# Kernel optimization log

Hardware: AMD Instinct MI355X
Metric: run time of the kernel (lower is better)

## Reference

```python
import jax, jax.numpy as jnp
import numpy as np

N = 50000
E = 800000
IN = 128
HID = 32
OUT = 32
H1, H2 = 4, 4
NEG_SLOPE = 0.2


def setup_inputs() -> dict:
    key = jax.random.key(0)
    ks = jax.random.split(key, 12)
    x = jax.random.normal(ks[0], (N, IN), dtype=jnp.float32)
    src = jax.random.randint(ks[1], (E,), 0, N, dtype=jnp.int32)
    dst = jax.random.randint(ks[2], (E,), 0, N, dtype=jnp.int32)
    s = 0.1
    # layer 1: fc (IN -> H1*HID, no bias), attn vectors (H1, HID), bias (H1*HID,)
    W1 = jax.random.normal(ks[3], (IN, H1 * HID), dtype=jnp.float32) * s
    al1 = jax.random.normal(ks[4], (H1, HID), dtype=jnp.float32) * s
    ar1 = jax.random.normal(ks[5], (H1, HID), dtype=jnp.float32) * s
    b1 = jnp.zeros((H1 * HID,), dtype=jnp.float32)
    # layer 2: fc (H1*HID -> H2*OUT, no bias)
    W2 = jax.random.normal(ks[6], (H1 * HID, H2 * OUT), dtype=jnp.float32) * s
    al2 = jax.random.normal(ks[7], (H2, OUT), dtype=jnp.float32) * s
    ar2 = jax.random.normal(ks[8], (H2, OUT), dtype=jnp.float32) * s
    b2 = jnp.zeros((H2 * OUT,), dtype=jnp.float32)
    return {"x": x, "W1": W1, "al1": al1, "ar1": ar1, "b1": b1,
            "W2": W2, "al2": al2, "ar2": ar2, "b2": b2,
            "src": src, "dst": dst}


def _gat_layer(x, W, al, ar, b, src, dst, n, h, d):
    # feat_drop is identity (eval mode)
    feat = (x @ W).reshape(n, h, d)                       # [N,H,D]
    el = jnp.einsum('nhd,hd->nh', feat, al)               # [N,H]
    er = jnp.einsum('nhd,hd->nh', feat, ar)               # [N,H]
    e = jax.nn.leaky_relu(el[src] + er[dst], NEG_SLOPE)   # [E,H] SDDMM
    # edge softmax over incoming edges of each destination node
    emax = jax.ops.segment_max(e, dst, num_segments=n)    # [N,H]
    emax = jnp.where(jnp.isfinite(emax), emax, 0.0)       # guard 0-in-degree
    w = jnp.exp(e - emax[dst])                            # [E,H]
    denom = jax.ops.segment_sum(w, dst, num_segments=n)   # [N,H]
    alpha = w / jnp.maximum(denom[dst], 1e-9)             # [E,H]; attn_drop identity
    # SpMM aggregation
    rst = jax.ops.segment_sum(feat[src] * alpha[:, :, None], dst, num_segments=n)
    # residual: in_feats == h*d for both layers -> DGL uses Identity res_fc
    rst = rst + x.reshape(n, h, d)
    rst = rst + b.reshape(1, h, d)
    return rst


def reference(x, W1, al1, ar1, b1, W2, al2, ar2, b2, src, dst):
    h = _gat_layer(x, W1, al1, ar1, b1, src, dst, N, H1, HID)
    h = jax.nn.elu(h)                                     # layer-1 activation
    h = h.reshape(N, H1 * HID)                            # flatten(1)
    h = _gat_layer(h, W2, al2, ar2, b2, src, dst, N, H2, OUT)
    return h.mean(axis=1)                                 # [N,OUT]
```

## Files before the change

kernel.cpp:

```cpp
#include <hip/hip_runtime.h>
#include <cstdint>
#include <cstddef>

#define NEG_SLOPE 0.2f

typedef __bf16 bf16x8 __attribute__((ext_vector_type(8)));
typedef float  f32x4  __attribute__((ext_vector_type(4)));

__device__ inline unsigned int bf16pair(float a, float b) {
    unsigned int ua = __float_as_uint(a), ub = __float_as_uint(b);
    ua += 0x7fffu + ((ua >> 16) & 1u);
    ub += 0x7fffu + ((ub >> 16) & 1u);
    return (ua >> 16) | (ub & 0xffff0000u);
}
__device__ inline unsigned short bf16r(float x) {
    unsigned int u = __float_as_uint(x);
    u += 0x7fffu + ((u >> 16) & 1u);
    return (unsigned short)(u >> 16);
}

__global__ __launch_bounds__(256) void prep_kernel(
    const float* __restrict__ W1, const float* __restrict__ W2,
    unsigned short* __restrict__ Wt1, unsigned short* __restrict__ Wt2,
    const int* __restrict__ dst, int* __restrict__ deg,
    int* __restrict__ rank, int E)
{
    __shared__ float tile[64][65];
    if (blockIdx.x < 8) {
        const float* W = (blockIdx.x < 4) ? W1 : W2;
        unsigned short* Wt = (blockIdx.x < 4) ? Wt1 : Wt2;
        const int tb = blockIdx.x & 3;
        const int k0 = (tb >> 1) * 64, n0 = (tb & 1) * 64;
        const int c = threadIdx.x & 63, r4 = threadIdx.x >> 6;
#pragma unroll
        for (int i = 0; i < 16; ++i) {
            const int r = i * 4 + r4;
            tile[r][c] = W[(size_t)(k0 + r) * 128 + n0 + c];
        }
        __syncthreads();
#pragma unroll
        for (int i = 0; i < 16; ++i) {
            const int nn = i * 4 + r4;
            Wt[(size_t)(n0 + nn) * 128 + k0 + c] = bf16r(tile[c][nn]);
        }
        return;
    }
    const int bid = blockIdx.x - 8;
    const int e4 = (bid * 256 + threadIdx.x) * 4;
    if (e4 + 4 <= E) {
        const int4 d = *(const int4*)&dst[e4];
        int4 r;
        r.x = atomicAdd(&deg[d.x], 1);
        r.y = atomicAdd(&deg[d.y], 1);
        r.z = atomicAdd(&deg[d.z], 1);
        r.w = atomicAdd(&deg[d.w], 1);
        *(int4*)&rank[e4] = r;
    } else {
        for (int e = e4; e < E; ++e) rank[e] = atomicAdd(&deg[dst[e]], 1);
    }
}

template <bool XBF16>
__global__ __launch_bounds__(256, 4) void gemm_attn_kernel(
    const void* __restrict__ Xv, const unsigned short* __restrict__ Wt,
    const float* __restrict__ al, const float* __restrict__ ar,
    unsigned short* __restrict__ feat16, float* __restrict__ el,
    float* __restrict__ er, int n)
{
    __shared__ unsigned short sX[64][136];
    __shared__ unsigned short sF[64][136];

    const int t = threadIdx.x;
    const int rowbase = blockIdx.x * 64;

    if (XBF16) {
        const unsigned short* X = (const unsigned short*)Xv;
#pragma unroll
        for (int i = 0; i < 4; ++i) {
            const int idx = t + 256 * i;
            const int row = idx >> 4;
            const int q   = idx & 15;
            int g = rowbase + row; if (g >= n) g = n - 1;
            *(uint4*)&sX[row][q * 8] = *(const uint4*)&X[(size_t)g * 128 + q * 8];
        }
    } else {
        const float* X = (const float*)Xv;
#pragma unroll
        for (int i = 0; i < 8; ++i) {
            const int idx = t + 256 * i;
            const int row = idx >> 5;
            const int kq  = (idx & 31) * 4;
            int g = rowbase + row; if (g >= n) g = n - 1;
            const float4 v = *(const float4*)&X[(size_t)g * 128 + kq];
            uint2 pk;
            pk.x = bf16pair(v.x, v.y);
            pk.y = bf16pair(v.z, v.w);
            *(uint2*)&sX[row][kq] = pk;
        }
    }

    const int lane = t & 63;
    const int w    = t >> 6;
    const int m    = lane & 15;
    const int g4   = lane >> 4;

    bf16x8 bfr[2][4];
#pragma unroll
    for (int tile = 0; tile < 2; ++tile)
#pragma unroll
        for (int ks = 0; ks < 4; ++ks)
            bfr[tile][ks] = *(const bf16x8*)
                &Wt[(size_t)(w * 32 + tile * 16 + m) * 128 + ks * 32 + g4 * 8];

    __syncthreads();

    const int n0 = w * 32 + m, n1 = n0 + 16;
    const float al0 = al[n0], ar0 = ar[n0];
    const float al1 = al[n1], ar1 = ar[n1];
    const int swz = g4 << 3;

#pragma unroll
    for (int rt = 0; rt < 4; ++rt) {
        bf16x8 a[4];
#pragma unroll
        for (int ks = 0; ks < 4; ++ks)
            a[ks] = *(const bf16x8*)&sX[rt * 16 + m][ks * 32 + g4 * 8];
        f32x4 acc0 = {0.f, 0.f, 0.f, 0.f}, acc1 = {0.f, 0.f, 0.f, 0.f};
#pragma unroll
        for (int ks = 0; ks < 4; ++ks) {
            acc0 = __builtin_amdgcn_mfma_f32_16x16x32_bf16(a[ks], bfr[0][ks], acc0, 0, 0, 0);
            acc1 = __builtin_amdgcn_mfma_f32_16x16x32_bf16(a[ks], bfr[1][ks], acc1, 0, 0, 0);
        }
#pragma unroll
        for (int r = 0; r < 4; ++r) {
            const int row = rt * 16 + g4 * 4 + r;
            sF[row][(n0) ^ swz]      = bf16r(acc0[r]);
            sF[row][(n1) ^ swz]      = bf16r(acc1[r]);
            float pl = acc0[r] * al0 + acc1[r] * al1;
            float pr = acc0[r] * ar0 + acc1[r] * ar1;
            pl += __shfl_xor(pl, 1); pr += __shfl_xor(pr, 1);
            pl += __shfl_xor(pl, 2); pr += __shfl_xor(pr, 2);
            pl += __shfl_xor(pl, 4); pr += __shfl_xor(pr, 4);
            pl += __shfl_xor(pl, 8); pr += __shfl_xor(pr, 8);
            if (m == 0 && rowbase + row < n) {
                el[(size_t)(rowbase + row) * 4 + w] = pl;
                er[(size_t)(rowbase + row) * 4 + w] = pr;
            }
        }
    }

    __syncthreads();
    {
        const int row = t >> 2;
        const int q   = t & 3;
        const int g   = rowbase + row;
        const int sw_ = ((row >> 2) & 3) << 3;
        if (g < n) {
#pragma unroll
            for (int i = 0; i < 4; ++i) {
                const int c0 = q * 8 + i * 32;
                *(uint4*)&feat16[(size_t)g * 128 + c0] =
                    *(const uint4*)&sF[row][c0 ^ sw_];
            }
        }
    }
}

__global__ __launch_bounds__(1024) void scan_kernel(
    const int* __restrict__ deg, int* __restrict__ off, int n)
{
    __shared__ int wsums[16];
    __shared__ int s_carry;
    const int tid  = threadIdx.x;
    const int lane = tid & 63;
    const int wid  = tid >> 6;

    if (tid == 0) { s_carry = 0; off[0] = 0; }
    __syncthreads();

    const int n4 = n >> 2;
    const int4* __restrict__ deg4 = (const int4*)deg;

    for (int base = 0; base < n4; base += 1024) {
        const int i4 = base + tid;
        int4 v = make_int4(0, 0, 0, 0);
        if (i4 < n4) v = deg4[i4];
        const int t0 = v.x, t1 = t0 + v.y, t2 = t1 + v.z, t3 = t2 + v.w;

        int x = t3;
#pragma unroll
        for (int d = 1; d < 64; d <<= 1) {
            int y = __shfl_up(x, d);
            if (lane >= d) x += y;
        }
        if (lane == 63) wsums[wid] = x;
        __syncthreads();

        if (wid == 0 && lane < 16) {
            int xx = wsums[lane];
#pragma unroll
            for (int d = 1; d < 16; d <<= 1) {
                int y = __shfl_up(xx, d);
                if (lane >= d) xx += y;
            }
            wsums[lane] = xx;
        }
        __syncthreads();

        const int wp   = (wid == 0) ? 0 : wsums[wid - 1];
        const int excl = s_carry + wp + (x - t3);
        if (i4 < n4) {
            off[4 * i4 + 1] = excl + t0;
            off[4 * i4 + 2] = excl + t1;
            off[4 * i4 + 3] = excl + t2;
            off[4 * i4 + 4] = excl + t3;
        }
        __syncthreads();
        if (tid == 0) s_carry += wsums[15];
        __syncthreads();
    }
}

__global__ void place_kernel(const int* __restrict__ src, const int* __restrict__ dst,
                             const int* __restrict__ off, const int* __restrict__ rank,
                             int* __restrict__ csr_src, int E)
{
    const int e4 = (blockIdx.x * blockDim.x + threadIdx.x) * 4;
    if (e4 + 4 <= E) {
        const int4 s = *(const int4*)&src[e4];
        const int4 d = *(const int4*)&dst[e4];
        const int4 r = *(const int4*)&rank[e4];
        const int o0 = off[d.x], o1 = off[d.y], o2 = off[d.z], o3 = off[d.w];
        csr_src[o0 + r.x] = s.x;
        csr_src[o1 + r.y] = s.y;
        csr_src[o2 + r.z] = s.z;
        csr_src[o3 + r.w] = s.w;
    } else {
        for (int e = e4; e < E; ++e)
            csr_src[off[dst[e]] + rank[e]] = src[e];
    }
}

template <bool LAYER2>
__global__ __launch_bounds__(256) void agg_kernel(
    const int* __restrict__ off, const int* __restrict__ csr_src,
    const unsigned short* __restrict__ feat16, const float* __restrict__ el,
    const float* __restrict__ er, const void* __restrict__ resid,
    const float* __restrict__ bias, void* __restrict__ out, int n)
{
    const int lane = threadIdx.x & 63;
    const int node = blockIdx.x * 4 + (threadIdx.x >> 6);
    if (node >= n) return;

    const int h  = lane >> 4;
    const int d0 = 2 * lane;

    const float erh = er[(size_t)node * 4 + h];
    const unsigned int* __restrict__ fb = (const unsigned int*)feat16;

    const int beg = off[node], end = off[node + 1];

    float acc0 = 0.f, acc1 = 0.f, sw = 0.f;
    int j = beg;

    for (; j + 16 <= end; j += 16) {
        int s[16]; float ev[16]; unsigned int uv[16];
#pragma unroll
        for (int q = 0; q < 16; ++q) s[q] = csr_src[j + q];
#pragma unroll
        for (int q = 0; q < 16; ++q) ev[q] = el[(size_t)s[q] * 4 + h];
#pragma unroll
        for (int q = 0; q < 16; ++q) uv[q] = fb[(size_t)s[q] * 64 + lane];
#pragma unroll
        for (int q = 0; q < 16; ++q) {
            float a = ev[q] + erh;
            a = fmaxf(a, NEG_SLOPE * a);
            const float wq = __expf(a);
            acc0 += wq * __uint_as_float(uv[q] << 16);
            acc1 += wq * __uint_as_float(uv[q] & 0xffff0000u);
            sw += wq;
        }
    }
    for (; j + 4 <= end; j += 4) {
        int s[4]; float ev[4]; unsigned int uv[4];
#pragma unroll
        for (int q = 0; q < 4; ++q) s[q] = csr_src[j + q];
#pragma unroll
        for (int q = 0; q < 4; ++q) ev[q] = el[(size_t)s[q] * 4 + h];
#pragma unroll
        for (int q = 0; q < 4; ++q) uv[q] = fb[(size_t)s[q] * 64 + lane];
#pragma unroll
        for (int q = 0; q < 4; ++q) {
            float a = ev[q] + erh;
            a = fmaxf(a, NEG_SLOPE * a);
            const float wq = __expf(a);
            acc0 += wq * __uint_as_float(uv[q] << 16);
            acc1 += wq * __uint_as_float(uv[q] & 0xffff0000u);
            sw += wq;
        }
    }
    for (; j < end; ++j) {
        const int s = csr_src[j];
        float a = el[(size_t)s * 4 + h] + erh;
        a = fmaxf(a, NEG_SLOPE * a);
        const float wq = __expf(a);
        const unsigned int u = fb[(size_t)s * 64 + lane];
        acc0 += wq * __uint_as_float(u << 16);
        acc1 += wq * __uint_as_float(u & 0xffff0000u);
        sw += wq;
    }

    const float inv = 1.f / fmaxf(sw, 1e-9f);
    float rx, ry;
    if (!LAYER2) {
        const float2 rs = *(const float2*)((const float*)resid + (size_t)node * 128 + d0);
        rx = rs.x; ry = rs.y;
    } else {
        const unsigned int u =
            *(const unsigned int*)((const unsigned short*)resid + (size_t)node * 128 + d0);
        rx = __uint_as_float(u << 16);
        ry = __uint_as_float(u & 0xffff0000u);
    }
    float v0 = acc0 * inv + rx + bias[d0];
    float v1 = acc1 * inv + ry + bias[d0 + 1];

    if (!LAYER2) {
        v0 = (v0 > 0.f) ? v0 : expm1f(v0);
        v1 = (v1 > 0.f) ? v1 : expm1f(v1);
        *(unsigned int*)((unsigned short*)out + (size_t)node * 128 + d0) = bf16pair(v0, v1);
    } else {
        float s0 = v0, s1 = v1;
        s0 += __shfl_xor(s0, 16); s1 += __shfl_xor(s1, 16);
        s0 += __shfl_xor(s0, 32); s1 += __shfl_xor(s1, 32);
        if (lane < 16)
            *(float2*)((float*)out + (size_t)node * 32 + 2 * lane) =
                make_float2(s0 * 0.25f, s1 * 0.25f);
    }
}

extern "C" void kernel_launch(void* const* d_in, const int* in_sizes, int n_in,
                              void* d_out, int out_size, void* d_ws, size_t ws_size,
                              hipStream_t stream)
{
    const float* x   = (const float*)d_in[0];
    const float* W1  = (const float*)d_in[1];
    const float* al1 = (const float*)d_in[2];
    const float* ar1 = (const float*)d_in[3];
    const float* b1  = (const float*)d_in[4];
    const float* W2  = (const float*)d_in[5];
    const float* al2 = (const float*)d_in[6];
    const float* ar2 = (const float*)d_in[7];
    const float* b2  = (const float*)d_in[8];
    const int*   src = (const int*)d_in[9];
    const int*   dst = (const int*)d_in[10];

    const int n = in_sizes[0] / 128;
    const int E = in_sizes[9];
    float* out = (float*)d_out;

    char* p = (char*)d_ws;
    unsigned short* h1b    = (unsigned short*)p; p += (size_t)n * 128 * sizeof(unsigned short);
    unsigned short* feat16 = (unsigned short*)p; p += (size_t)n * 128 * sizeof(unsigned short);
    float* el    = (float*)p;          p += (size_t)n * 4 * sizeof(float);
    float* er    = (float*)p;          p += (size_t)n * 4 * sizeof(float);
    int* off     = (int*)p;            p += (size_t)(n + 1) * sizeof(int);
    int* deg     = (int*)p;            p += (size_t)n * sizeof(int);
    int* rank    = (int*)p;            p += (size_t)E * sizeof(int);
    int* csr     = (int*)p;            p += (size_t)E * sizeof(int);
    unsigned short* wt1 = (unsigned short*)p; p += (size_t)128 * 128 * sizeof(unsigned short);
    unsigned short* wt2 = (unsigned short*)p; p += (size_t)128 * 128 * sizeof(unsigned short);

    hipMemsetAsync(deg, 0, (size_t)n * sizeof(int), stream);

    const int gemm_grid  = (n + 63) / 64;
    const int edge4_grid = (E / 4 + 255) / 256;
    const int agg_grid   = (n + 3) / 4;

    prep_kernel<<<8 + edge4_grid, 256, 0, stream>>>(W1, W2, wt1, wt2, dst, deg, rank, E);
    gemm_attn_kernel<false><<<gemm_grid, 256, 0, stream>>>(x, wt1, al1, ar1, feat16, el, er, n);
    scan_kernel<<<1, 1024, 0, stream>>>(deg, off, n);
    place_kernel<<<edge4_grid, 256, 0, stream>>>(src, dst, off, rank, csr, E);
    agg_kernel<false><<<agg_grid, 256, 0, stream>>>(off, csr, feat16, el, er, x, b1, h1b, n);
    gemm_attn_kernel<true><<<gemm_grid, 256, 0, stream>>>(h1b, wt2, al2, ar2, feat16, el, er, n);
    agg_kernel<true><<<agg_grid, 256, 0, stream>>>(off, csr, feat16, el, er, h1b, b2, out, n);
}
```

Measured before the change: 282.5 us.

## Distribute edge weight computation across lanes and broadcast via shuffles in aggregation

```diff
diff --git a/kernel.cpp b/kernel.cpp
--- a/kernel.cpp
+++ b/kernel.cpp
@@ -134,8 +134,8 @@
 #pragma unroll
         for (int r = 0; r < 4; ++r) {
             const int row = rt * 16 + g4 * 4 + r;
-            sF[row][(n0) ^ swz]      = bf16r(acc0[r]);
-            sF[row][(n1) ^ swz]      = bf16r(acc1[r]);
+            sF[row][(n0) ^ swz] = bf16r(acc0[r]);
+            sF[row][(n1) ^ swz] = bf16r(acc1[r]);
             float pl = acc0[r] * al0 + acc1[r] * al1;
             float pr = acc0[r] * ar0 + acc1[r] * ar1;
             pl += __shfl_xor(pl, 1); pr += __shfl_xor(pr, 1);
@@ -252,63 +252,52 @@
     const int node = blockIdx.x * 4 + (threadIdx.x >> 6);
     if (node >= n) return;
 
-    const int h  = lane >> 4;
-    const int d0 = 2 * lane;
+    const int h   = lane >> 4;
+    const int qid = lane & 15;
+    const int d0  = 2 * lane;
 
     const float erh = er[(size_t)node * 4 + h];
     const unsigned int* __restrict__ fb = (const unsigned int*)feat16;
 
     const int beg = off[node], end = off[node + 1];
 
-    float acc0 = 0.f, acc1 = 0.f, sw = 0.f;
-    int j = beg;
-
-    for (; j + 16 <= end; j += 16) {
-        int s[16]; float ev[16]; unsigned int uv[16];
-#pragma unroll
-        for (int q = 0; q < 16; ++q) s[q] = csr_src[j + q];
-#pragma unroll
-        for (int q = 0; q < 16; ++q) ev[q] = el[(size_t)s[q] * 4 + h];
-#pragma unroll
-        for (int q = 0; q < 16; ++q) uv[q] = fb[(size_t)s[q] * 64 + lane];
-#pragma unroll
-        for (int q = 0; q < 16; ++q) {
-            float a = ev[q] + erh;
-            a = fmaxf(a, NEG_SLOPE * a);
-            const float wq = __expf(a);
-            acc0 += wq * __uint_as_float(uv[q] << 16);
-            acc1 += wq * __uint_as_float(uv[q] & 0xffff0000u);
-            sw += wq;
-        }
-    }
-    for (; j + 4 <= end; j += 4) {
-        int s[4]; float ev[4]; unsigned int uv[4];
-#pragma unroll
-        for (int q = 0; q < 4; ++q) s[q] = csr_src[j + q];
-#pragma unroll
-        for (int q = 0; q < 4; ++q) ev[q] = el[(size_t)s[q] * 4 + h];
-#pragma unroll
-        for (int q = 0; q < 4; ++q) uv[q] = fb[(size_t)s[q] * 64 + lane];
-#pragma unroll
-        for (int q = 0; q < 4; ++q) {
-            float a = ev[q] + erh;
-            a = fmaxf(a, NEG_SLOPE * a);
-            const float wq = __expf(a);
-            acc0 += wq * __uint_as_float(uv[q] << 16);
-            acc1 += wq * __uint_as_float(uv[q] & 0xffff0000u);
-            sw += wq;
-        }
-    }
-    for (; j < end; ++j) {
-        const int s = csr_src[j];
-        float a = el[(size_t)s * 4 + h] + erh;
+    float acc0 = 0.f, acc1 = 0.f, swacc = 0.f;
+
+    for (int j = beg; j < end; j += 16) {
+        const int rem = end - j;
+        const int myq = (qid < rem) ? qid : 0;
+        const int sl  = csr_src[j + myq];
+        float a = el[(size_t)sl * 4 + h] + erh;
         a = fmaxf(a, NEG_SLOPE * a);
-        const float wq = __expf(a);
-        const unsigned int u = fb[(size_t)s * 64 + lane];
-        acc0 += wq * __uint_as_float(u << 16);
-        acc1 += wq * __uint_as_float(u & 0xffff0000u);
-        sw += wq;
-    }
+        float wl = __expf(a);
+        if (qid >= rem) wl = 0.f;
+        swacc += wl;
+
+        if (rem >= 16) {
+#pragma unroll
+            for (int q = 0; q < 16; ++q) {
+                const int   sq = __shfl(sl, q);
+                const float wq = __shfl(wl, (lane & 48) + q);
+                const unsigned int u = fb[(size_t)sq * 64 + lane];
+                acc0 += wq * __uint_as_float(u << 16);
+                acc1 += wq * __uint_as_float(u & 0xffff0000u);
+            }
+        } else {
+            for (int q = 0; q < rem; ++q) {
+                const int   sq = __shfl(sl, q);
+                const float wq = __shfl(wl, (lane & 48) + q);
+                const unsigned int u = fb[(size_t)sq * 64 + lane];
+                acc0 += wq * __uint_as_float(u << 16);
+                acc1 += wq * __uint_as_float(u & 0xffff0000u);
+            }
+        }
+    }
+
+    float sw = swacc;
+    sw += __shfl_xor(sw, 1);
+    sw += __shfl_xor(sw, 2);
+    sw += __shfl_xor(sw, 4);
+    sw += __shfl_xor(sw, 8);
 
     const float inv = 1.f / fmaxf(sw, 1e-9f);
     float rx, ry;
```

Measured after the change: 294.8 us. 4.3% more time.

## Precompute edge attention weights in CSR placement kernel before aggregation

Applied to the files above, without the earlier changes.

```diff
diff --git a/kernel.cpp b/kernel.cpp
--- a/kernel.cpp
+++ b/kernel.cpp
@@ -134,8 +134,8 @@
 #pragma unroll
         for (int r = 0; r < 4; ++r) {
             const int row = rt * 16 + g4 * 4 + r;
-            sF[row][(n0) ^ swz]      = bf16r(acc0[r]);
-            sF[row][(n1) ^ swz]      = bf16r(acc1[r]);
+            sF[row][(n0) ^ swz] = bf16r(acc0[r]);
+            sF[row][(n1) ^ swz] = bf16r(acc1[r]);
             float pl = acc0[r] * al0 + acc1[r] * al1;
             float pr = acc0[r] * ar0 + acc1[r] * ar1;
             pl += __shfl_xor(pl, 1); pr += __shfl_xor(pr, 1);
@@ -223,30 +223,57 @@
 
 __global__ void place_kernel(const int* __restrict__ src, const int* __restrict__ dst,
                              const int* __restrict__ off, const int* __restrict__ rank,
-                             int* __restrict__ csr_src, int E)
+                             const float* __restrict__ el, const float* __restrict__ er,
+                             int* __restrict__ csr_src, float* __restrict__ csr_w, int E)
 {
     const int e4 = (blockIdx.x * blockDim.x + threadIdx.x) * 4;
     if (e4 + 4 <= E) {
         const int4 s = *(const int4*)&src[e4];
         const int4 d = *(const int4*)&dst[e4];
         const int4 r = *(const int4*)&rank[e4];
-        const int o0 = off[d.x], o1 = off[d.y], o2 = off[d.z], o3 = off[d.w];
-        csr_src[o0 + r.x] = s.x;
-        csr_src[o1 + r.y] = s.y;
-        csr_src[o2 + r.z] = s.z;
-        csr_src[o3 + r.w] = s.w;
+        const int p0 = off[d.x] + r.x, p1 = off[d.y] + r.y;
+        const int p2 = off[d.z] + r.z, p3 = off[d.w] + r.w;
+        csr_src[p0] = s.x; csr_src[p1] = s.y;
+        csr_src[p2] = s.z; csr_src[p3] = s.w;
+        const int sv[4] = {s.x, s.y, s.z, s.w};
+        const int dv[4] = {d.x, d.y, d.z, d.w};
+        const int pv[4] = {p0, p1, p2, p3};
+#pragma unroll
+        for (int k = 0; k < 4; ++k) {
+            const float4 e_l = *(const float4*)&el[(size_t)sv[k] * 4];
+            const float4 e_r = *(const float4*)&er[(size_t)dv[k] * 4];
+            float4 wv;
+            float a;
+            a = e_l.x + e_r.x; a = fmaxf(a, NEG_SLOPE * a); wv.x = __expf(a);
+            a = e_l.y + e_r.y; a = fmaxf(a, NEG_SLOPE * a); wv.y = __expf(a);
+            a = e_l.z + e_r.z; a = fmaxf(a, NEG_SLOPE * a); wv.z = __expf(a);
+            a = e_l.w + e_r.w; a = fmaxf(a, NEG_SLOPE * a); wv.w = __expf(a);
+            *(float4*)&csr_w[(size_t)pv[k] * 4] = wv;
+        }
     } else {
-        for (int e = e4; e < E; ++e)
-            csr_src[off[dst[e]] + rank[e]] = src[e];
+        for (int e = e4; e < E; ++e) {
+            const int sv = src[e], dv = dst[e];
+            const int pos = off[dv] + rank[e];
+            csr_src[pos] = sv;
+            const float4 e_l = *(const float4*)&el[(size_t)sv * 4];
+            const float4 e_r = *(const float4*)&er[(size_t)dv * 4];
+            float4 wv;
+            float a;
+            a = e_l.x + e_r.x; a = fmaxf(a, NEG_SLOPE * a); wv.x = __expf(a);
+            a = e_l.y + e_r.y; a = fmaxf(a, NEG_SLOPE * a); wv.y = __expf(a);
+            a = e_l.z + e_r.z; a = fmaxf(a, NEG_SLOPE * a); wv.z = __expf(a);
+            a = e_l.w + e_r.w; a = fmaxf(a, NEG_SLOPE * a); wv.w = __expf(a);
+            *(float4*)&csr_w[(size_t)pos * 4] = wv;
+        }
     }
 }
 
 template <bool LAYER2>
 __global__ __launch_bounds__(256) void agg_kernel(
     const int* __restrict__ off, const int* __restrict__ csr_src,
-    const unsigned short* __restrict__ feat16, const float* __restrict__ el,
-    const float* __restrict__ er, const void* __restrict__ resid,
-    const float* __restrict__ bias, void* __restrict__ out, int n)
+    const float* __restrict__ csr_w, const unsigned short* __restrict__ feat16,
+    const void* __restrict__ resid, const float* __restrict__ bias,
+    void* __restrict__ out, int n)
 {
     const int lane = threadIdx.x & 63;
     const int node = blockIdx.x * 4 + (threadIdx.x >> 6);
@@ -255,7 +282,6 @@
     const int h  = lane >> 4;
     const int d0 = 2 * lane;
 
-    const float erh = er[(size_t)node * 4 + h];
     const unsigned int* __restrict__ fb = (const unsigned int*)feat16;
 
     const int beg = off[node], end = off[node + 1];
@@ -264,46 +290,38 @@
     int j = beg;
 
     for (; j + 16 <= end; j += 16) {
-        int s[16]; float ev[16]; unsigned int uv[16];
+        int s[16]; float wv[16]; unsigned int uv[16];
 #pragma unroll
         for (int q = 0; q < 16; ++q) s[q] = csr_src[j + q];
 #pragma unroll
-        for (int q = 0; q < 16; ++q) ev[q] = el[(size_t)s[q] * 4 + h];
+        for (int q = 0; q < 16; ++q) wv[q] = csr_w[(size_t)(j + q) * 4 + h];
 #pragma unroll
         for (int q = 0; q < 16; ++q) uv[q] = fb[(size_t)s[q] * 64 + lane];
 #pragma unroll
         for (int q = 0; q < 16; ++q) {
-            float a = ev[q] + erh;
-            a = fmaxf(a, NEG_SLOPE * a);
-            const float wq = __expf(a);
-            acc0 += wq * __uint_as_float(uv[q] << 16);
-            acc1 += wq * __uint_as_float(uv[q] & 0xffff0000u);
-            sw += wq;
+            acc0 += wv[q] * __uint_as_float(uv[q] << 16);
+            acc1 += wv[q] * __uint_as_float(uv[q] & 0xffff0000u);
+            sw += wv[q];
         }
     }
     for (; j + 4 <= end; j += 4) {
-        int s[4]; float ev[4]; unsigned int uv[4];
+        int s[4]; float wv[4]; unsigned int uv[4];
 #pragma unroll
         for (int q = 0; q < 4; ++q) s[q] = csr_src[j + q];
 #pragma unroll
-        for (int q = 0; q < 4; ++q) ev[q] = el[(size_t)s[q] * 4 + h];
+        for (int q = 0; q < 4; ++q) wv[q] = csr_w[(size_t)(j + q) * 4 + h];
 #pragma unroll
         for (int q = 0; q < 4; ++q) uv[q] = fb[(size_t)s[q] * 64 + lane];
 #pragma unroll
         for (int q = 0; q < 4; ++q) {
-            float a = ev[q] + erh;
-            a = fmaxf(a, NEG_SLOPE * a);
-            const float wq = __expf(a);
-            acc0 += wq * __uint_as_float(uv[q] << 16);
-            acc1 += wq * __uint_as_float(uv[q] & 0xffff0000u);
-            sw += wq;
+            acc0 += wv[q] * __uint_as_float(uv[q] << 16);
+            acc1 += wv[q] * __uint_as_float(uv[q] & 0xffff0000u);
+            sw += wv[q];
         }
     }
     for (; j < end; ++j) {
         const int s = csr_src[j];
-        float a = el[(size_t)s * 4 + h] + erh;
-        a = fmaxf(a, NEG_SLOPE * a);
-        const float wq = __expf(a);
+        const float wq = csr_w[(size_t)j * 4 + h];
         const unsigned int u = fb[(size_t)s * 64 + lane];
         acc0 += wq * __uint_as_float(u << 16);
         acc1 += wq * __uint_as_float(u & 0xffff0000u);
@@ -367,6 +385,7 @@
     int* deg     = (int*)p;            p += (size_t)n * sizeof(int);
     int* rank    = (int*)p;            p += (size_t)E * sizeof(int);
     int* csr     = (int*)p;            p += (size_t)E * sizeof(int);
+    float* csr_w = (float*)p;          p += (size_t)E * 4 * sizeof(float);
     unsigned short* wt1 = (unsigned short*)p; p += (size_t)128 * 128 * sizeof(unsigned short);
     unsigned short* wt2 = (unsigned short*)p; p += (size_t)128 * 128 * sizeof(unsigned short);
 
@@ -379,8 +398,9 @@
     prep_kernel<<<8 + edge4_grid, 256, 0, stream>>>(W1, W2, wt1, wt2, dst, deg, rank, E);
     gemm_attn_kernel<false><<<gemm_grid, 256, 0, stream>>>(x, wt1, al1, ar1, feat16, el, er, n);
     scan_kernel<<<1, 1024, 0, stream>>>(deg, off, n);
-    place_kernel<<<edge4_grid, 256, 0, stream>>>(src, dst, off, rank, csr, E);
-    agg_kernel<false><<<agg_grid, 256, 0, stream>>>(off, csr, feat16, el, er, x, b1, h1b, n);
+    place_kernel<<<edge4_grid, 256, 0, stream>>>(src, dst, off, rank, el, er, csr, csr_w, E);
+    agg_kernel<false><<<agg_grid, 256, 0, stream>>>(off, csr, csr_w, feat16, x, b1, h1b, n);
     gemm_attn_kernel<true><<<gemm_grid, 256, 0, stream>>>(h1b, wt2, al2, ar2, feat16, el, er, n);
-    agg_kernel<true><<<agg_grid, 256, 0, stream>>>(off, csr, feat16, el, er, h1b, b2, out, n);
-}
+    place_kernel<<<edge4_grid, 256, 0, stream>>>(src, dst, off, rank, el, er, csr, csr_w, E);
+    agg_kernel<true><<<agg_grid, 256, 0, stream>>>(off, csr, csr_w, feat16, h1b, b2, out, n);
+}
```

Result: slower. 338.6 us (+19.9%).

## Fuse layer-1 aggregation with layer-2 GEMM and attention into one kernel

Applied to the files above, without the earlier changes.

```diff
diff --git a/kernel.cpp b/kernel.cpp
--- a/kernel.cpp
+++ b/kernel.cpp
@@ -60,9 +60,8 @@
     }
 }
 
-template <bool XBF16>
 __global__ __launch_bounds__(256, 4) void gemm_attn_kernel(
-    const void* __restrict__ Xv, const unsigned short* __restrict__ Wt,
+    const float* __restrict__ X, const unsigned short* __restrict__ Wt,
     const float* __restrict__ al, const float* __restrict__ ar,
     unsigned short* __restrict__ feat16, float* __restrict__ el,
     float* __restrict__ er, int n)
@@ -73,30 +72,17 @@
     const int t = threadIdx.x;
     const int rowbase = blockIdx.x * 64;
 
-    if (XBF16) {
-        const unsigned short* X = (const unsigned short*)Xv;
-#pragma unroll
-        for (int i = 0; i < 4; ++i) {
-            const int idx = t + 256 * i;
-            const int row = idx >> 4;
-            const int q   = idx & 15;
-            int g = rowbase + row; if (g >= n) g = n - 1;
-            *(uint4*)&sX[row][q * 8] = *(const uint4*)&X[(size_t)g * 128 + q * 8];
-        }
-    } else {
-        const float* X = (const float*)Xv;
-#pragma unroll
-        for (int i = 0; i < 8; ++i) {
-            const int idx = t + 256 * i;
-            const int row = idx >> 5;
-            const int kq  = (idx & 31) * 4;
-            int g = rowbase + row; if (g >= n) g = n - 1;
-            const float4 v = *(const float4*)&X[(size_t)g * 128 + kq];
-            uint2 pk;
-            pk.x = bf16pair(v.x, v.y);
-            pk.y = bf16pair(v.z, v.w);
-            *(uint2*)&sX[row][kq] = pk;
-        }
+#pragma unroll
+    for (int i = 0; i < 8; ++i) {
+        const int idx = t + 256 * i;
+        const int row = idx >> 5;
+        const int kq  = (idx & 31) * 4;
+        int g = rowbase + row; if (g >= n) g = n - 1;
+        const float4 v = *(const float4*)&X[(size_t)g * 128 + kq];
+        uint2 pk;
+        pk.x = bf16pair(v.x, v.y);
+        pk.y = bf16pair(v.z, v.w);
+        *(uint2*)&sX[row][kq] = pk;
     }
 
     const int lane = t & 63;
@@ -134,8 +120,8 @@
 #pragma unroll
         for (int r = 0; r < 4; ++r) {
             const int row = rt * 16 + g4 * 4 + r;
-            sF[row][(n0) ^ swz]      = bf16r(acc0[r]);
-            sF[row][(n1) ^ swz]      = bf16r(acc1[r]);
+            sF[row][(n0) ^ swz] = bf16r(acc0[r]);
+            sF[row][(n1) ^ swz] = bf16r(acc1[r]);
             float pl = acc0[r] * al0 + acc1[r] * al1;
             float pr = acc0[r] * ar0 + acc1[r] * ar1;
             pl += __shfl_xor(pl, 1); pr += __shfl_xor(pr, 1);
@@ -241,12 +227,163 @@
     }
 }
 
-template <bool LAYER2>
-__global__ __launch_bounds__(256) void agg_kernel(
+__global__ __launch_bounds__(256, 4) void layer_kernel(
+    const int* __restrict__ off, const int* __restrict__ csr_src,
+    const unsigned short* __restrict__ feat1, const float* __restrict__ el1,
+    const float* __restrict__ er1, const float* __restrict__ x,
+    const float* __restrict__ b1, unsigned short* __restrict__ h1b,
+    const unsigned short* __restrict__ Wt2, const float* __restrict__ al2,
+    const float* __restrict__ ar2, unsigned short* __restrict__ feat2,
+    float* __restrict__ el2, float* __restrict__ er2, int n)
+{
+    __shared__ unsigned short sH[64][136];
+    __shared__ unsigned short sF[64][136];
+
+    const int t = threadIdx.x;
+    const int lane = t & 63;
+    const int w    = t >> 6;
+    const int rowbase = blockIdx.x * 64;
+
+    const int h  = lane >> 4;
+    const int d0 = 2 * lane;
+    const unsigned int* __restrict__ fb = (const unsigned int*)feat1;
+
+    for (int i = 0; i < 16; ++i) {
+        const int node = rowbase + w * 16 + i;
+        unsigned int pk = 0;
+        if (node < n) {
+            const float erh = er1[(size_t)node * 4 + h];
+            const int beg = off[node], end = off[node + 1];
+            float acc0 = 0.f, acc1 = 0.f, sw = 0.f;
+            int j = beg;
+            for (; j + 16 <= end; j += 16) {
+                int s[16]; float ev[16]; unsigned int uv[16];
+#pragma unroll
+                for (int q = 0; q < 16; ++q) s[q] = csr_src[j + q];
+#pragma unroll
+                for (int q = 0; q < 16; ++q) ev[q] = el1[(size_t)s[q] * 4 + h];
+#pragma unroll
+                for (int q = 0; q < 16; ++q) uv[q] = fb[(size_t)s[q] * 64 + lane];
+#pragma unroll
+                for (int q = 0; q < 16; ++q) {
+                    float a = ev[q] + erh;
+                    a = fmaxf(a, NEG_SLOPE * a);
+                    const float wq = __expf(a);
+                    acc0 += wq * __uint_as_float(uv[q] << 16);
+                    acc1 += wq * __uint_as_float(uv[q] & 0xffff0000u);
+                    sw += wq;
+                }
+            }
+            for (; j + 4 <= end; j += 4) {
+                int s[4]; float ev[4]; unsigned int uv[4];
+#pragma unroll
+                for (int q = 0; q < 4; ++q) s[q] = csr_src[j + q];
+#pragma unroll
+                for (int q = 0; q < 4; ++q) ev[q] = el1[(size_t)s[q] * 4 + h];
+#pragma unroll
+                for (int q = 0; q < 4; ++q) uv[q] = fb[(size_t)s[q] * 64 + lane];
+#pragma unroll
+                for (int q = 0; q < 4; ++q) {
+                    float a = ev[q] + erh;
+                    a = fmaxf(a, NEG_SLOPE * a);
+                    const float wq = __expf(a);
+                    acc0 += wq * __uint_as_float(uv[q] << 16);
+                    acc1 += wq * __uint_as_float(uv[q] & 0xffff0000u);
+                    sw += wq;
+                }
+            }
+            for (; j < end; ++j) {
+                const int s = csr_src[j];
+                float a = el1[(size_t)s * 4 + h] + erh;
+                a = fmaxf(a, NEG_SLOPE * a);
+                const float wq = __expf(a);
+                const unsigned int u = fb[(size_t)s * 64 + lane];
+                acc0 += wq * __uint_as_float(u << 16);
+                acc1 += wq * __uint_as_float(u & 0xffff0000u);
+                sw += wq;
+            }
+            const float inv = 1.f / fmaxf(sw, 1e-9f);
+            const float2 rs = *(const float2*)&x[(size_t)node * 128 + d0];
+            float v0 = acc0 * inv + rs.x + b1[d0];
+            float v1 = acc1 * inv + rs.y + b1[d0 + 1];
+            v0 = (v0 > 0.f) ? v0 : expm1f(v0);
+            v1 = (v1 > 0.f) ? v1 : expm1f(v1);
+            pk = bf16pair(v0, v1);
+            *(unsigned int*)&h1b[(size_t)node * 128 + d0] = pk;
+        }
+        *(unsigned int*)&sH[w * 16 + i][d0] = pk;
+    }
+
+    __syncthreads();
+
+    const int m  = lane & 15;
+    const int g4 = lane >> 4;
+
+    bf16x8 bfr[2][4];
+#pragma unroll
+    for (int tile = 0; tile < 2; ++tile)
+#pragma unroll
+        for (int ks = 0; ks < 4; ++ks)
+            bfr[tile][ks] = *(const bf16x8*)
+                &Wt2[(size_t)(w * 32 + tile * 16 + m) * 128 + ks * 32 + g4 * 8];
+
+    const int n0 = w * 32 + m, n1 = n0 + 16;
+    const float al0 = al2[n0], ar0 = ar2[n0];
+    const float al1 = al2[n1], ar1 = ar2[n1];
+    const int swz = g4 << 3;
+
+#pragma unroll
+    for (int rt = 0; rt < 4; ++rt) {
+        bf16x8 a[4];
+#pragma unroll
+        for (int ks = 0; ks < 4; ++ks)
+            a[ks] = *(const bf16x8*)&sH[rt * 16 + m][ks * 32 + g4 * 8];
+        f32x4 acc0 = {0.f, 0.f, 0.f, 0.f}, acc1 = {0.f, 0.f, 0.f, 0.f};
+#pragma unroll
+        for (int ks = 0; ks < 4; ++ks) {
+            acc0 = __builtin_amdgcn_mfma_f32_16x16x32_bf16(a[ks], bfr[0][ks], acc0, 0, 0, 0);
+            acc1 = __builtin_amdgcn_mfma_f32_16x16x32_bf16(a[ks], bfr[1][ks], acc1, 0, 0, 0);
+        }
+#pragma unroll
+        for (int r = 0; r < 4; ++r) {
+            const int row = rt * 16 + g4 * 4 + r;
+            sF[row][(n0) ^ swz] = bf16r(acc0[r]);
+            sF[row][(n1) ^ swz] = bf16r(acc1[r]);
+            float pl = acc0[r] * al0 + acc1[r] * al1;
+            float pr = acc0[r] * ar0 + acc1[r] * ar1;
+            pl += __shfl_xor(pl, 1); pr += __shfl_xor(pr, 1);
+            pl += __shfl_xor(pl, 2); pr += __shfl_xor(pr, 2);
+            pl += __shfl_xor(pl, 4); pr += __shfl_xor(pr, 4);
+            pl += __shfl_xor(pl, 8); pr += __shfl_xor(pr, 8);
+            if (m == 0 && rowbase + row < n) {
+                el2[(size_t)(rowbase + row) * 4 + w] = pl;
+                er2[(size_t)(rowbase + row) * 4 + w] = pr;
+            }
+        }
+    }
+
+    __syncthreads();
+    {
+        const int row = t >> 2;
+        const int q   = t & 3;
+        const int g   = rowbase + row;
+        const int sw_ = ((row >> 2) & 3) << 3;
+        if (g < n) {
+#pragma unroll
+            for (int i = 0; i < 4; ++i) {
+                const int c0 = q * 8 + i * 32;
+                *(uint4*)&feat2[(size_t)g * 128 + c0] =
+                    *(const uint4*)&sF[row][c0 ^ sw_];
+            }
+        }
+    }
+}
+
+__global__ __launch_bounds__(256) void agg2_kernel(
     const int* __restrict__ off, const int* __restrict__ csr_src,
     const unsigned short* __restrict__ feat16, const float* __restrict__ el,
-    const float* __restrict__ er, const void* __restrict__ resid,
-    const float* __restrict__ bias, void* __restrict__ out, int n)
+    const float* __restrict__ er, const unsigned short* __restrict__ resid,
+    const float* __restrict__ bias, float* __restrict__ out, int n)
 {
     const int lane = threadIdx.x & 63;
     const int node = blockIdx.x * 4 + (threadIdx.x >> 6);
@@ -311,31 +448,18 @@
     }
 
     const float inv = 1.f / fmaxf(sw, 1e-9f);
-    float rx, ry;
-    if (!LAYER2) {
-        const float2 rs = *(const float2*)((const float*)resid + (size_t)node * 128 + d0);
-        rx = rs.x; ry = rs.y;
-    } else {
-        const unsigned int u =
-            *(const unsigned int*)((const unsigned short*)resid + (size_t)node * 128 + d0);
-        rx = __uint_as_float(u << 16);
-        ry = __uint_as_float(u & 0xffff0000u);
-    }
+    const unsigned int u = *(const unsigned int*)&resid[(size_t)node * 128 + d0];
+    const float rx = __uint_as_float(u << 16);
+    const float ry = __uint_as_float(u & 0xffff0000u);
     float v0 = acc0 * inv + rx + bias[d0];
     float v1 = acc1 * inv + ry + bias[d0 + 1];
 
-    if (!LAYER2) {
-        v0 = (v0 > 0.f) ? v0 : expm1f(v0);
-        v1 = (v1 > 0.f) ? v1 : expm1f(v1);
-        *(unsigned int*)((unsigned short*)out + (size_t)node * 128 + d0) = bf16pair(v0, v1);
-    } else {
-        float s0 = v0, s1 = v1;
-        s0 += __shfl_xor(s0, 16); s1 += __shfl_xor(s1, 16);
-        s0 += __shfl_xor(s0, 32); s1 += __shfl_xor(s1, 32);
-        if (lane < 16)
-            *(float2*)((float*)out + (size_t)node * 32 + 2 * lane) =
-                make_float2(s0 * 0.25f, s1 * 0.25f);
-    }
+    float s0 = v0, s1 = v1;
+    s0 += __shfl_xor(s0, 16); s1 += __shfl_xor(s1, 16);
+    s0 += __shfl_xor(s0, 32); s1 += __shfl_xor(s1, 32);
+    if (lane < 16)
+        *(float2*)&out[(size_t)node * 32 + 2 * lane] =
+            make_float2(s0 * 0.25f, s1 * 0.25f);
 }
 
 extern "C" void kernel_launch(void* const* d_in, const int* in_sizes, int n_in,
@@ -359,10 +483,13 @@
     float* out = (float*)d_out;
 
     char* p = (char*)d_ws;
-    unsigned short* h1b    = (unsigned short*)p; p += (size_t)n * 128 * sizeof(unsigned short);
-    unsigned short* feat16 = (unsigned short*)p; p += (size_t)n * 128 * sizeof(unsigned short);
-    float* el    = (float*)p;          p += (size_t)n * 4 * sizeof(float);
-    float* er    = (float*)p;          p += (size_t)n * 4 * sizeof(float);
+    unsigned short* h1b   = (unsigned short*)p; p += (size_t)n * 128 * sizeof(unsigned short);
+    unsigned short* feat1 = (unsigned short*)p; p += (size_t)n * 128 * sizeof(unsigned short);
+    unsigned short* feat2 = (unsigned short*)p; p += (size_t)n * 128 * sizeof(unsigned short);
+    float* el1   = (float*)p;          p += (size_t)n * 4 * sizeof(float);
+    float* er1   = (float*)p;          p += (size_t)n * 4 * sizeof(float);
+    float* el2   = (float*)p;          p += (size_t)n * 4 * sizeof(float);
+    float* er2   = (float*)p;          p += (size_t)n * 4 * sizeof(float);
     int* off     = (int*)p;            p += (size_t)(n + 1) * sizeof(int);
     int* deg     = (int*)p;            p += (size_t)n * sizeof(int);
     int* rank    = (int*)p;            p += (size_t)E * sizeof(int);
@@ -377,10 +504,10 @@
     const int agg_grid   = (n + 3) / 4;
 
     prep_kernel<<<8 + edge4_grid, 256, 0, stream>>>(W1, W2, wt1, wt2, dst, deg, rank, E);
-    gemm_attn_kernel<false><<<gemm_grid, 256, 0, stream>>>(x, wt1, al1, ar1, feat16, el, er, n);
+    gemm_attn_kernel<<<gemm_grid, 256, 0, stream>>>(x, wt1, al1, ar1, feat1, el1, er1, n);
     scan_kernel<<<1, 1024, 0, stream>>>(deg, off, n);
     place_kernel<<<edge4_grid, 256, 0, stream>>>(src, dst, off, rank, csr, E);
-    agg_kernel<false><<<agg_grid, 256, 0, stream>>>(off, csr, feat16, el, er, x, b1, h1b, n);
-    gemm_attn_kernel<true><<<gemm_grid, 256, 0, stream>>>(h1b, wt2, al2, ar2, feat16, el, er, n);
-    agg_kernel<true><<<agg_grid, 256, 0, stream>>>(off, csr, feat16, el, er, h1b, b2, out, n);
-}
+    layer_kernel<<<gemm_grid, 256, 0, stream>>>(off, csr, feat1, el1, er1, x, b1, h1b,
+                                                wt2, al2, ar2, feat2, el2, er2, n);
+    agg2_kernel<<<agg_grid, 256, 0, stream>>>(off, csr, feat2, el2, er2, h1b, b2, out, n);
+}
```

New measurement: 293.1 us. 1.04x slower.
